# Optimization experiments

Measured on AMD Instinct MI355X. Metric: run time of the kernel, lower is better.

The kernel has to match this reference:

```python
import jax, jax.numpy as jnp
import numpy as np

TEMPERATURE = 0.07
NEG_INF_FILL = -1e9  # matches torch fill_diagonal_(-1000000000.0)


def setup_inputs() -> dict:
    key = jax.random.key(0)
    feats = jax.random.normal(key, (6144, 768), dtype=jnp.float32)
    return {"feats": feats}


def reference(feats):
    # L2-normalize rows (torch F.normalize uses eps=1e-12 clamp on the norm)
    norm = jnp.maximum(jnp.linalg.norm(feats, axis=1, keepdims=True), 1e-12)
    f = feats / norm
    N = f.shape[0]
    sim = jnp.matmul(f, f.T) / TEMPERATURE            # [N, N]
    eye = jnp.eye(N, dtype=bool)
    sim = jnp.where(eye, NEG_INF_FILL, sim)           # fill diagonal
    labels = jnp.arange(N) // 3                       # 3 views per slice
    pos = (labels[:, None] == labels[None, :]) & ~eye  # positives, self excluded
    # masked logsumexp over positives via weights b (grad-safe masking)
    numerator = jax.scipy.special.logsumexp(sim, axis=1, b=pos.astype(sim.dtype))
    denominator = jax.scipy.special.logsumexp(sim, axis=1)
    loss = jnp.sum(-(numerator - denominator)) / N
    return loss
```

## Files before the change

kernel.cpp:

```cpp
#include <hip/hip_runtime.h>

#define NN 6144
#define DD 768
#define NGROUP 2048
#define NB 48
#define NTILES 1176
#define INV_T 14.285714285714286f
#define CMAX  14.285714285714286f

typedef __bf16 bf16x4_t __attribute__((ext_vector_type(4)));
typedef __bf16 bf16x8_t __attribute__((ext_vector_type(8)));
typedef float f32x4_t __attribute__((ext_vector_type(4)));

__device__ __forceinline__ void load_lds16(const void* g, void* l) {
    __builtin_amdgcn_global_load_lds((__attribute__((address_space(1))) void*)g,
                                     (__attribute__((address_space(3))) void*)l,
                                     16, 0, 0);
}

__global__ void norm_num_kernel(const float* __restrict__ feats,
                                __bf16* __restrict__ fb,
                                float* __restrict__ num,
                                float* __restrict__ den_sum) {
    const int wid = threadIdx.x >> 6;
    const int lane = threadIdx.x & 63;
    const int g = blockIdx.x * 4 + wid;
    const int r0 = g * 3;

    if (threadIdx.x < 12) den_sum[blockIdx.x * 12 + threadIdx.x] = 0.0f;

    const float4* A = (const float4*)(feats + (size_t)r0 * DD);
    const float4* B = (const float4*)(feats + (size_t)(r0 + 1) * DD);
    const float4* C = (const float4*)(feats + (size_t)(r0 + 2) * DD);

    float4 va[3], vb[3], vc[3];
    float ss0 = 0.f, ss1 = 0.f, ss2 = 0.f, d01 = 0.f, d02 = 0.f, d12 = 0.f;
#pragma unroll
    for (int i = 0; i < 3; ++i) {
        va[i] = A[lane + i * 64];
        vb[i] = B[lane + i * 64];
        vc[i] = C[lane + i * 64];
        ss0 += va[i].x * va[i].x + va[i].y * va[i].y + va[i].z * va[i].z + va[i].w * va[i].w;
        ss1 += vb[i].x * vb[i].x + vb[i].y * vb[i].y + vb[i].z * vb[i].z + vb[i].w * vb[i].w;
        ss2 += vc[i].x * vc[i].x + vc[i].y * vc[i].y + vc[i].z * vc[i].z + vc[i].w * vc[i].w;
        d01 += va[i].x * vb[i].x + va[i].y * vb[i].y + va[i].z * vb[i].z + va[i].w * vb[i].w;
        d02 += va[i].x * vc[i].x + va[i].y * vc[i].y + va[i].z * vc[i].z + va[i].w * vc[i].w;
        d12 += vb[i].x * vc[i].x + vb[i].y * vc[i].y + vb[i].z * vc[i].z + vb[i].w * vc[i].w;
    }
#pragma unroll
    for (int m = 32; m >= 1; m >>= 1) {
        ss0 += __shfl_xor(ss0, m);
        ss1 += __shfl_xor(ss1, m);
        ss2 += __shfl_xor(ss2, m);
        d01 += __shfl_xor(d01, m);
        d02 += __shfl_xor(d02, m);
        d12 += __shfl_xor(d12, m);
    }
    const float s0 = 1.0f / fmaxf(sqrtf(ss0), 1e-12f);
    const float s1 = 1.0f / fmaxf(sqrtf(ss1), 1e-12f);
    const float s2 = 1.0f / fmaxf(sqrtf(ss2), 1e-12f);

#pragma unroll
    for (int i = 0; i < 3; ++i) {
        bf16x4_t o0, o1, o2;
        o0[0] = (__bf16)(va[i].x * s0); o0[1] = (__bf16)(va[i].y * s0);
        o0[2] = (__bf16)(va[i].z * s0); o0[3] = (__bf16)(va[i].w * s0);
        o1[0] = (__bf16)(vb[i].x * s1); o1[1] = (__bf16)(vb[i].y * s1);
        o1[2] = (__bf16)(vb[i].z * s1); o1[3] = (__bf16)(vb[i].w * s1);
        o2[0] = (__bf16)(vc[i].x * s2); o2[1] = (__bf16)(vc[i].y * s2);
        o2[2] = (__bf16)(vc[i].z * s2); o2[3] = (__bf16)(vc[i].w * s2);
        const size_t cofs = (size_t)(lane + i * 64) * 4;
        *(bf16x4_t*)(fb + (size_t)r0 * DD + cofs) = o0;
        *(bf16x4_t*)(fb + (size_t)(r0 + 1) * DD + cofs) = o1;
        *(bf16x4_t*)(fb + (size_t)(r0 + 2) * DD + cofs) = o2;
    }

    if (lane == 0) {
        const float s01 = d01 * s0 * s1 * INV_T;
        const float s02 = d02 * s0 * s2 * INV_T;
        const float s12 = d12 * s1 * s2 * INV_T;
        num[r0]     = fmaxf(s01, s02) + log1pf(__expf(-fabsf(s01 - s02)));
        num[r0 + 1] = fmaxf(s01, s12) + log1pf(__expf(-fabsf(s01 - s12)));
        num[r0 + 2] = fmaxf(s02, s12) + log1pf(__expf(-fabsf(s02 - s12)));
    }
}

__global__ __launch_bounds__(256, 5) void gemm_expsum_kernel(
        const __bf16* __restrict__ fb, float* __restrict__ den_sum) {
    __shared__ __bf16 sA[128 * 64];
    __shared__ __bf16 sB[128 * 64];

    int rem = blockIdx.x;
    int bi = 0, rowlen = NB;
    while (rem >= rowlen) { rem -= rowlen; rowlen--; bi++; }
    const int bj = bi + rem;
    const bool isdiag = (bi == bj);
    const int i0 = bi * 128;
    const int j0 = bj * 128;

    const int t = threadIdx.x;
    const int lane = t & 63;
    const int wid = t >> 6;
    const int wm = wid >> 1;
    const int wn = wid & 1;

    const int srow = t >> 3;
    const int scol = ((t & 7) ^ (srow & 7)) * 8;
    const __bf16* gA = fb + (size_t)(i0 + srow) * DD + scol;
    const __bf16* gB = fb + (size_t)(j0 + srow) * DD + scol;
    __bf16* ldsA = sA + (size_t)((wid << 6) * 8);
    __bf16* ldsB = sB + (size_t)((wid << 6) * 8);

    f32x4_t acc[4][4];
    const f32x4_t zz = {0.0f, 0.0f, 0.0f, 0.0f};
#pragma unroll
    for (int mi = 0; mi < 4; ++mi)
#pragma unroll
        for (int ni = 0; ni < 4; ++ni) acc[mi][ni] = zz;

    for (int kb = 0; kb < 12; ++kb) {
        const int k0 = kb * 64;
#pragma unroll
        for (int i = 0; i < 4; ++i) {
            load_lds16(gA + (size_t)(i * 32) * DD + k0, ldsA + (size_t)(i * 256) * 8);
            load_lds16(gB + (size_t)(i * 32) * DD + k0, ldsB + (size_t)(i * 256) * 8);
        }
        __syncthreads();
#pragma unroll
        for (int kk = 0; kk < 2; ++kk) {
            const int kx = (((lane >> 4) + kk * 4) ^ (lane & 7)) * 8;
            bf16x8_t af[4], bfr[4];
#pragma unroll
            for (int mi = 0; mi < 4; ++mi)
                af[mi] = *(const bf16x8_t*)&sA[(wm * 64 + mi * 16 + (lane & 15)) * 64 + kx];
#pragma unroll
            for (int ni = 0; ni < 4; ++ni)
                bfr[ni] = *(const bf16x8_t*)&sB[(wn * 64 + ni * 16 + (lane & 15)) * 64 + kx];
#pragma unroll
            for (int mi = 0; mi < 4; ++mi)
#pragma unroll
                for (int ni = 0; ni < 4; ++ni)
                    acc[mi][ni] = __builtin_amdgcn_mfma_f32_16x16x32_bf16(
                        af[mi], bfr[ni], acc[mi][ni], 0, 0, 0);
        }
        __syncthreads();
    }

    const int colb = j0 + wn * 64 + (lane & 15);
    const int rowb = i0 + wm * 64 + ((lane >> 4) << 2);
    float cs[4] = {0.f, 0.f, 0.f, 0.f};
#pragma unroll
    for (int mi = 0; mi < 4; ++mi) {
        float rsv[4] = {0.f, 0.f, 0.f, 0.f};
#pragma unroll
        for (int ni = 0; ni < 4; ++ni) {
            const int col = colb + ni * 16;
#pragma unroll
            for (int r = 0; r < 4; ++r) {
                const int row = rowb + mi * 16 + r;
                const float v = acc[mi][ni][r] * INV_T;
                float e = __expf(v - CMAX);
                if (isdiag && row == col) e = 0.0f;
                rsv[r] += e;
                cs[ni] += e;
            }
        }
#pragma unroll
        for (int r = 0; r < 4; ++r) {
            float v = rsv[r];
            v += __shfl_xor(v, 8);
            v += __shfl_xor(v, 4);
            v += __shfl_xor(v, 2);
            v += __shfl_xor(v, 1);
            if ((lane & 15) == 0) atomicAdd(&den_sum[rowb + mi * 16 + r], v);
        }
    }
    if (!isdiag) {
#pragma unroll
        for (int ni = 0; ni < 4; ++ni) {
            float v = cs[ni];
            v += __shfl_xor(v, 16);
            v += __shfl_xor(v, 32);
            if ((lane >> 4) == 0) atomicAdd(&den_sum[colb + ni * 16], v);
        }
    }
}

__global__ void finalize_kernel(const float* __restrict__ den_sum,
                                const float* __restrict__ num,
                                float* __restrict__ out) {
    float local = 0.0f;
    for (int i = threadIdx.x; i < NN; i += 256) {
        local += logf(den_sum[i]) + CMAX - num[i];
    }
#pragma unroll
    for (int m = 32; m >= 1; m >>= 1) local += __shfl_xor(local, m);
    __shared__ float ws[4];
    if ((threadIdx.x & 63) == 0) ws[threadIdx.x >> 6] = local;
    __syncthreads();
    if (threadIdx.x == 0) out[0] = (ws[0] + ws[1] + ws[2] + ws[3]) / (float)NN;
}

extern "C" void kernel_launch(void* const* d_in, const int* in_sizes, int n_in,
                              void* d_out, int out_size, void* d_ws, size_t ws_size,
                              hipStream_t stream) {
    const float* feats = (const float*)d_in[0];
    float* out = (float*)d_out;

    char* ws = (char*)d_ws;
    __bf16* fb     = (__bf16*)ws;
    float* num     = (float*)(ws + 9437184);
    float* den_sum = (float*)(ws + 9437184 + 24576);

    norm_num_kernel<<<NGROUP / 4, 256, 0, stream>>>(feats, fb, num, den_sum);
    gemm_expsum_kernel<<<NTILES, 256, 0, stream>>>(fb, den_sum);
    finalize_kernel<<<1, 256, 0, stream>>>(den_sum, num, out);
}
```

Before: 127.7 us.

## Switch Gram GEMM to FP8 scaled MFMA and compute positives inside GEMM epilogue

Normalized features are now stored as FP8 (e4m3) instead of bf16, and the GEMM uses the 16x16x128 f8f6f4 scaled MFMA with K-tiles of 128 bytes. This halves the feature traffic and the LDS footprint per k-step, and uses the higher-throughput FP8 matrix path. The numerator is no longer computed in the norm kernel; the GEMM epilogue on near-diagonal tiles accumulates positive-pair exponentials, and finalize takes the log of that sum. FP8 loses precision in the similarities, which are scaled by 1/T, so the loss may drift from the reference.

```diff
diff --git a/kernel.cpp b/kernel.cpp
--- a/kernel.cpp
+++ b/kernel.cpp
@@ -2,14 +2,13 @@
 
 #define NN 6144
 #define DD 768
-#define NGROUP 2048
 #define NB 48
 #define NTILES 1176
 #define INV_T 14.285714285714286f
 #define CMAX  14.285714285714286f
 
-typedef __bf16 bf16x4_t __attribute__((ext_vector_type(4)));
-typedef __bf16 bf16x8_t __attribute__((ext_vector_type(8)));
+typedef int i32x4 __attribute__((ext_vector_type(4)));
+typedef int i32x8 __attribute__((ext_vector_type(8)));
 typedef float f32x4_t __attribute__((ext_vector_type(4)));
 
 __device__ __forceinline__ void load_lds16(const void* g, void* l) {
@@ -18,83 +17,48 @@
                                      16, 0, 0);
 }
 
-__global__ void norm_num_kernel(const float* __restrict__ feats,
-                                __bf16* __restrict__ fb,
-                                float* __restrict__ num,
-                                float* __restrict__ den_sum) {
+__global__ void norm_kernel(const float* __restrict__ feats,
+                            unsigned int* __restrict__ fb8,
+                            float* __restrict__ den_num) {
     const int wid = threadIdx.x >> 6;
     const int lane = threadIdx.x & 63;
-    const int g = blockIdx.x * 4 + wid;
-    const int r0 = g * 3;
-
-    if (threadIdx.x < 12) den_sum[blockIdx.x * 12 + threadIdx.x] = 0.0f;
-
-    const float4* A = (const float4*)(feats + (size_t)r0 * DD);
-    const float4* B = (const float4*)(feats + (size_t)(r0 + 1) * DD);
-    const float4* C = (const float4*)(feats + (size_t)(r0 + 2) * DD);
-
-    float4 va[3], vb[3], vc[3];
-    float ss0 = 0.f, ss1 = 0.f, ss2 = 0.f, d01 = 0.f, d02 = 0.f, d12 = 0.f;
+    const int row = blockIdx.x * 4 + wid;
+
+    if (threadIdx.x < 8) den_num[blockIdx.x * 8 + threadIdx.x] = 0.0f;
+
+    const float4* src = (const float4*)(feats + (size_t)row * DD);
+    float4 v[3];
+    float ss = 0.0f;
 #pragma unroll
     for (int i = 0; i < 3; ++i) {
-        va[i] = A[lane + i * 64];
-        vb[i] = B[lane + i * 64];
-        vc[i] = C[lane + i * 64];
-        ss0 += va[i].x * va[i].x + va[i].y * va[i].y + va[i].z * va[i].z + va[i].w * va[i].w;
-        ss1 += vb[i].x * vb[i].x + vb[i].y * vb[i].y + vb[i].z * vb[i].z + vb[i].w * vb[i].w;
-        ss2 += vc[i].x * vc[i].x + vc[i].y * vc[i].y + vc[i].z * vc[i].z + vc[i].w * vc[i].w;
-        d01 += va[i].x * vb[i].x + va[i].y * vb[i].y + va[i].z * vb[i].z + va[i].w * vb[i].w;
-        d02 += va[i].x * vc[i].x + va[i].y * vc[i].y + va[i].z * vc[i].z + va[i].w * vc[i].w;
-        d12 += vb[i].x * vc[i].x + vb[i].y * vc[i].y + vb[i].z * vc[i].z + vb[i].w * vc[i].w;
-    }
-#pragma unroll
-    for (int m = 32; m >= 1; m >>= 1) {
-        ss0 += __shfl_xor(ss0, m);
-        ss1 += __shfl_xor(ss1, m);
-        ss2 += __shfl_xor(ss2, m);
-        d01 += __shfl_xor(d01, m);
-        d02 += __shfl_xor(d02, m);
-        d12 += __shfl_xor(d12, m);
-    }
-    const float s0 = 1.0f / fmaxf(sqrtf(ss0), 1e-12f);
-    const float s1 = 1.0f / fmaxf(sqrtf(ss1), 1e-12f);
-    const float s2 = 1.0f / fmaxf(sqrtf(ss2), 1e-12f);
+        v[i] = src[lane + i * 64];
+        ss += v[i].x * v[i].x + v[i].y * v[i].y + v[i].z * v[i].z + v[i].w * v[i].w;
+    }
+#pragma unroll
+    for (int m = 32; m >= 1; m >>= 1) ss += __shfl_xor(ss, m);
+    const float sc = 1.0f / fmaxf(sqrtf(ss), 1e-12f);
 
 #pragma unroll
     for (int i = 0; i < 3; ++i) {
-        bf16x4_t o0, o1, o2;
-        o0[0] = (__bf16)(va[i].x * s0); o0[1] = (__bf16)(va[i].y * s0);
-        o0[2] = (__bf16)(va[i].z * s0); o0[3] = (__bf16)(va[i].w * s0);
-        o1[0] = (__bf16)(vb[i].x * s1); o1[1] = (__bf16)(vb[i].y * s1);
-        o1[2] = (__bf16)(vb[i].z * s1); o1[3] = (__bf16)(vb[i].w * s1);
-        o2[0] = (__bf16)(vc[i].x * s2); o2[1] = (__bf16)(vc[i].y * s2);
-        o2[2] = (__bf16)(vc[i].z * s2); o2[3] = (__bf16)(vc[i].w * s2);
-        const size_t cofs = (size_t)(lane + i * 64) * 4;
-        *(bf16x4_t*)(fb + (size_t)r0 * DD + cofs) = o0;
-        *(bf16x4_t*)(fb + (size_t)(r0 + 1) * DD + cofs) = o1;
-        *(bf16x4_t*)(fb + (size_t)(r0 + 2) * DD + cofs) = o2;
-    }
-
-    if (lane == 0) {
-        const float s01 = d01 * s0 * s1 * INV_T;
-        const float s02 = d02 * s0 * s2 * INV_T;
-        const float s12 = d12 * s1 * s2 * INV_T;
-        num[r0]     = fmaxf(s01, s02) + log1pf(__expf(-fabsf(s01 - s02)));
-        num[r0 + 1] = fmaxf(s01, s12) + log1pf(__expf(-fabsf(s01 - s12)));
-        num[r0 + 2] = fmaxf(s02, s12) + log1pf(__expf(-fabsf(s02 - s12)));
-    }
-}
-
-__global__ __launch_bounds__(256, 5) void gemm_expsum_kernel(
-        const __bf16* __restrict__ fb, float* __restrict__ den_sum) {
-    __shared__ __bf16 sA[128 * 64];
-    __shared__ __bf16 sB[128 * 64];
+        unsigned int w = 0;
+        w = __builtin_amdgcn_cvt_pk_fp8_f32(v[i].x * sc, v[i].y * sc, w, 0);
+        w = __builtin_amdgcn_cvt_pk_fp8_f32(v[i].z * sc, v[i].w * sc, w, 1);
+        fb8[(size_t)row * 192 + lane + i * 64] = w;
+    }
+}
+
+__global__ __launch_bounds__(256, 4) void gemm_expsum_kernel(
+        const unsigned char* __restrict__ fb8,
+        float* __restrict__ den_sum, float* __restrict__ num_sum) {
+    __shared__ __align__(16) char sA[128 * 128];
+    __shared__ __align__(16) char sB[128 * 128];
 
     int rem = blockIdx.x;
     int bi = 0, rowlen = NB;
     while (rem >= rowlen) { rem -= rowlen; rowlen--; bi++; }
     const int bj = bi + rem;
     const bool isdiag = (bi == bj);
+    const bool neardiag = (bj - bi) <= 1;
     const int i0 = bi * 128;
     const int j0 = bj * 128;
 
@@ -105,11 +69,11 @@
     const int wn = wid & 1;
 
     const int srow = t >> 3;
-    const int scol = ((t & 7) ^ (srow & 7)) * 8;
-    const __bf16* gA = fb + (size_t)(i0 + srow) * DD + scol;
-    const __bf16* gB = fb + (size_t)(j0 + srow) * DD + scol;
-    __bf16* ldsA = sA + (size_t)((wid << 6) * 8);
-    __bf16* ldsB = sB + (size_t)((wid << 6) * 8);
+    const int scb = ((t & 7) ^ (srow & 7)) * 16;
+    const unsigned char* gA = fb8 + (size_t)(i0 + srow) * DD + scb;
+    const unsigned char* gB = fb8 + (size_t)(j0 + srow) * DD + scb;
+    char* ldsA = sA + wid * 1024;
+    char* ldsB = sB + wid * 1024;
 
     f32x4_t acc[4][4];
     const f32x4_t zz = {0.0f, 0.0f, 0.0f, 0.0f};
@@ -118,40 +82,52 @@
 #pragma unroll
         for (int ni = 0; ni < 4; ++ni) acc[mi][ni] = zz;
 
-    for (int kb = 0; kb < 12; ++kb) {
-        const int k0 = kb * 64;
+    const int q = lane >> 4;
+    const int mrow = lane & 15;
+    const int x7 = lane & 7;
+    const int c0 = ((q << 1) ^ x7) << 4;
+    const int c1 = (((q << 1) | 1) ^ x7) << 4;
+
+    for (int kb = 0; kb < 6; ++kb) {
+        const int k0 = kb * 128;
 #pragma unroll
         for (int i = 0; i < 4; ++i) {
-            load_lds16(gA + (size_t)(i * 32) * DD + k0, ldsA + (size_t)(i * 256) * 8);
-            load_lds16(gB + (size_t)(i * 32) * DD + k0, ldsB + (size_t)(i * 256) * 8);
+            load_lds16(gA + (size_t)(i * 32) * DD + k0, ldsA + i * 4096);
+            load_lds16(gB + (size_t)(i * 32) * DD + k0, ldsB + i * 4096);
         }
         __syncthreads();
-#pragma unroll
-        for (int kk = 0; kk < 2; ++kk) {
-            const int kx = (((lane >> 4) + kk * 4) ^ (lane & 7)) * 8;
-            bf16x8_t af[4], bfr[4];
+
+        i32x8 af[4];
+#pragma unroll
+        for (int mi = 0; mi < 4; ++mi) {
+            const char* p = sA + (wm * 64 + mi * 16 + mrow) * 128;
+            i32x4 lo = *(const i32x4*)(p + c0);
+            i32x4 hi = *(const i32x4*)(p + c1);
+            af[mi] = __builtin_shufflevector(lo, hi, 0, 1, 2, 3, 4, 5, 6, 7);
+        }
+#pragma unroll
+        for (int ni = 0; ni < 4; ++ni) {
+            const char* p = sB + (wn * 64 + ni * 16 + mrow) * 128;
+            i32x4 lo = *(const i32x4*)(p + c0);
+            i32x4 hi = *(const i32x4*)(p + c1);
+            i32x8 bf = __builtin_shufflevector(lo, hi, 0, 1, 2, 3, 4, 5, 6, 7);
 #pragma unroll
             for (int mi = 0; mi < 4; ++mi)
-                af[mi] = *(const bf16x8_t*)&sA[(wm * 64 + mi * 16 + (lane & 15)) * 64 + kx];
-#pragma unroll
-            for (int ni = 0; ni < 4; ++ni)
-                bfr[ni] = *(const bf16x8_t*)&sB[(wn * 64 + ni * 16 + (lane & 15)) * 64 + kx];
-#pragma unroll
-            for (int mi = 0; mi < 4; ++mi)
-#pragma unroll
-                for (int ni = 0; ni < 4; ++ni)
-                    acc[mi][ni] = __builtin_amdgcn_mfma_f32_16x16x32_bf16(
-                        af[mi], bfr[ni], acc[mi][ni], 0, 0, 0);
+                acc[mi][ni] = __builtin_amdgcn_mfma_scale_f32_16x16x128_f8f6f4(
+                    af[mi], bf, acc[mi][ni], 0, 0,
+                    0, 0x7F7F7F7F, 0, 0x7F7F7F7F);
         }
         __syncthreads();
     }
 
-    const int colb = j0 + wn * 64 + (lane & 15);
-    const int rowb = i0 + wm * 64 + ((lane >> 4) << 2);
+    const int colb = j0 + wn * 64 + mrow;
+    const int rowb = i0 + wm * 64 + (q << 2);
     float cs[4] = {0.f, 0.f, 0.f, 0.f};
+    float csn[4] = {0.f, 0.f, 0.f, 0.f};
 #pragma unroll
     for (int mi = 0; mi < 4; ++mi) {
         float rsv[4] = {0.f, 0.f, 0.f, 0.f};
+        float rsn[4] = {0.f, 0.f, 0.f, 0.f};
 #pragma unroll
         for (int ni = 0; ni < 4; ++ni) {
             const int col = colb + ni * 16;
@@ -163,6 +139,10 @@
                 if (isdiag && row == col) e = 0.0f;
                 rsv[r] += e;
                 cs[ni] += e;
+                if (neardiag && (row / 3 == col / 3) && row != col) {
+                    rsn[r] += e;
+                    csn[ni] += e;
+                }
             }
         }
 #pragma unroll
@@ -172,7 +152,18 @@
             v += __shfl_xor(v, 4);
             v += __shfl_xor(v, 2);
             v += __shfl_xor(v, 1);
-            if ((lane & 15) == 0) atomicAdd(&den_sum[rowb + mi * 16 + r], v);
+            if (mrow == 0) atomicAdd(&den_sum[rowb + mi * 16 + r], v);
+        }
+        if (neardiag) {
+#pragma unroll
+            for (int r = 0; r < 4; ++r) {
+                float v = rsn[r];
+                v += __shfl_xor(v, 8);
+                v += __shfl_xor(v, 4);
+                v += __shfl_xor(v, 2);
+                v += __shfl_xor(v, 1);
+                if (mrow == 0) atomicAdd(&num_sum[rowb + mi * 16 + r], v);
+            }
         }
     }
     if (!isdiag) {
@@ -181,17 +172,26 @@
             float v = cs[ni];
             v += __shfl_xor(v, 16);
             v += __shfl_xor(v, 32);
-            if ((lane >> 4) == 0) atomicAdd(&den_sum[colb + ni * 16], v);
+            if (q == 0) atomicAdd(&den_sum[colb + ni * 16], v);
+        }
+        if (neardiag) {
+#pragma unroll
+            for (int ni = 0; ni < 4; ++ni) {
+                float v = csn[ni];
+                v += __shfl_xor(v, 16);
+                v += __shfl_xor(v, 32);
+                if (q == 0) atomicAdd(&num_sum[colb + ni * 16], v);
+            }
         }
     }
 }
 
 __global__ void finalize_kernel(const float* __restrict__ den_sum,
-                                const float* __restrict__ num,
+                                const float* __restrict__ num_sum,
                                 float* __restrict__ out) {
     float local = 0.0f;
     for (int i = threadIdx.x; i < NN; i += 256) {
-        local += logf(den_sum[i]) + CMAX - num[i];
+        local += logf(den_sum[i]) - logf(num_sum[i]);
     }
 #pragma unroll
     for (int m = 32; m >= 1; m >>= 1) local += __shfl_xor(local, m);
@@ -208,11 +208,13 @@
     float* out = (float*)d_out;
 
     char* ws = (char*)d_ws;
-    __bf16* fb     = (__bf16*)ws;
-    float* num     = (float*)(ws + 9437184);
-    float* den_sum = (float*)(ws + 9437184 + 24576);
-
-    norm_num_kernel<<<NGROUP / 4, 256, 0, stream>>>(feats, fb, num, den_sum);
-    gemm_expsum_kernel<<<NTILES, 256, 0, stream>>>(fb, den_sum);
-    finalize_kernel<<<1, 256, 0, stream>>>(den_sum, num, out);
-}
+    unsigned int* fb8 = (unsigned int*)ws;
+    float* den_num    = (float*)(ws + 4718592);
+    float* den_sum    = den_num;
+    float* num_sum    = den_num + NN;
+
+    norm_kernel<<<NN / 4, 256, 0, stream>>>(feats, fb8, den_num);
+    gemm_expsum_kernel<<<NTILES, 256, 0, stream>>>((const unsigned char*)fb8,
+                                                   den_sum, num_sum);
+    finalize_kernel<<<1, 256, 0, stream>>>(den_sum, num_sum, out);
+}
```

Measured after the change: 348.0 us. +172.6%, slower.
